# Kernel tuning notes

Hardware: AMD Instinct MI355X
Metric: run time of the kernel (lower is better)

The kernel has to match this reference:

```python
import jax, jax.numpy as jnp
import numpy as np

IN_DIM, H_DIM, EMB_DIM, CHEB_K = 2, 64, 10, 3
B, L, N = 16, 12, 2048
CAT = IN_DIM + H_DIM


def setup_inputs() -> dict:
    key = jax.random.key(0)
    ks = jax.random.split(key, 7)
    x = jax.random.normal(ks[0], (B, L, N, IN_DIM), dtype=jnp.float32)
    node_embs = jax.random.normal(ks[1], (N, EMB_DIM), dtype=jnp.float32)
    As = jax.random.uniform(ks[2], (N, N), dtype=jnp.float32) / N  # row-stochastic-ish support
    # NAPL parameter pools (AGCRN-style): per-gate weight/bias pools indexed by node embedding
    s = 0.1
    Wg_pool = jax.random.normal(ks[3], (EMB_DIM, CHEB_K, CAT, 2 * H_DIM), dtype=jnp.float32) * s
    bg_pool = jax.random.normal(ks[4], (EMB_DIM, 2 * H_DIM), dtype=jnp.float32) * s
    Wc_pool = jax.random.normal(ks[5], (EMB_DIM, CHEB_K, CAT, H_DIM), dtype=jnp.float32) * s
    bc_pool = jax.random.normal(ks[6], (EMB_DIM, H_DIM), dtype=jnp.float32) * s
    return {"x": x, "node_embs": node_embs, "As": As,
            "Wg_pool": Wg_pool, "bg_pool": bg_pool,
            "Wc_pool": Wc_pool, "bc_pool": bc_pool}


def _cheb_supports(A, k):
    # T0 = I, T1 = A, T_j = 2 A T_{j-1} - T_{j-2}
    n = A.shape[0]
    Ts = [jnp.eye(n, dtype=A.dtype), A]
    for _ in range(2, k):
        Ts.append(2.0 * A @ Ts[-1] - Ts[-2])
    return jnp.stack(Ts[:k], axis=0)  # (K, N, N)


def _napl_conv(xin, supports, Wn, bn):
    # xin: (B,N,Ci); supports: (K,N,N); Wn: (N,K,Ci,Co); bn: (N,Co)
    xg = jnp.einsum('knm,bmc->bnkc', supports, xin)
    return jnp.einsum('bnki,nkio->bno', xg, Wn) + bn


def reference(x, node_embs, As, Wg_pool, bg_pool, Wc_pool, bc_pool):
    supports = _cheb_supports(As, CHEB_K)
    # node-adaptive parameters (time-invariant: hoist out of the recurrence)
    Wg = jnp.einsum('nd,dkio->nkio', node_embs, Wg_pool)  # (N,K,CAT,2H)
    bg = node_embs @ bg_pool                               # (N,2H)
    Wc = jnp.einsum('nd,dkio->nkio', node_embs, Wc_pool)  # (N,K,CAT,H)
    bc = node_embs @ bc_pool                               # (N,H)

    def step(h_prev, x_t):
        cat = jnp.concatenate([h_prev, x_t], axis=-1)      # (B,N,CAT)
        gate = jax.nn.sigmoid(_napl_conv(cat, supports, Wg, bg))
        r_t, u_t = jnp.split(gate, 2, axis=-1)
        cat2 = jnp.concatenate([r_t * h_prev, x_t], axis=-1)
        c_t = jnp.tanh(_napl_conv(cat2, supports, Wc, bc))
        h_t = u_t * h_prev + (1.0 - u_t) * c_t
        return h_t, h_t

    h0 = jnp.zeros((x.shape[0], x.shape[2], H_DIM), dtype=x.dtype)
    x_time = jnp.moveaxis(x, 1, 0)                          # (L,B,N,C)
    h_n, outs = jax.lax.scan(step, h0, x_time)
    output = jnp.moveaxis(outs, 0, 1)                       # (B,L,N,H)
    return output, h_n
```

## Files before the change

kernel.cpp:

```cpp
#include <hip/hip_runtime.h>
#include <cstdint>
#include <cstddef>

typedef _Float16 h16;
typedef h16 v8h __attribute__((ext_vector_type(8)));
typedef h16 v4h __attribute__((ext_vector_type(4)));
typedef float v4f __attribute__((ext_vector_type(4)));

constexpr int NN = 2048;
constexpr float INV_N = 1.0f / 2048.0f;
constexpr int LP = 72;

#define MFMA16(a, b, c) __builtin_amdgcn_mfma_f32_16x16x32_f16((a), (b), (c), 0, 0, 0)

__global__ void fill_k(float* __restrict__ o, float v, size_t ntot) {
  size_t i = (size_t)blockIdx.x * 256 + threadIdx.x;
  if (i < ntot) o[i] = v;
}


__global__ void prep_Asplit_k(const float* __restrict__ A,
                              h16* __restrict__ hi, h16* __restrict__ lo) {
  int tid = blockIdx.x * 256 + threadIdx.x;
  float v = A[tid] * 2048.0f;
  h16 h = (h16)v;
  hi[tid] = h;
  lo[tid] = (h16)(v - (float)h);
}

__global__ void prep_AsTsplit_k(const float* __restrict__ A,
                                h16* __restrict__ hi, h16* __restrict__ lo) {
  int tid = blockIdx.x * 256 + threadIdx.x;
  int t = tid & 2047, j = tid >> 11;
  float v = A[(size_t)t * NN + j] * 2048.0f;
  h16 h = (h16)v;
  hi[(size_t)j * NN + t] = h;
  lo[(size_t)j * NN + t] = (h16)(v - (float)h);
}

__global__ void prep_x0split_k(const float* __restrict__ x,
                               h16* __restrict__ hi, h16* __restrict__ lo) {
  int tid = blockIdx.x * 256 + threadIdx.x;
  int n = tid & 2047, c = tid >> 11;
  int ii = c & 1, b = (c >> 1) & 15, lt = c >> 5;
  float v = x[(((size_t)(b * 12 + lt)) * NN + n) * 2 + ii];
  h16 h = (h16)v;
  hi[tid] = h;
  lo[tid] = (h16)(v - (float)h);
}

template<int CO>
__global__ void prep_wts_k(const float* __restrict__ Wp,
                           h16* __restrict__ WTh, h16* __restrict__ WTl) {
  int tid = blockIdx.x * 256 + threadIdx.x;
  int kk = tid % 1920, o = tid / 1920;
  int d = kk / 192, rem = kk - d * 192;
  int jb = rem >> 6, i = rem & 63;
  float v;
  if (jb == 0)
    v = Wp[((size_t)((d * 3 + 0) * 66 + i)) * CO + o] -
        Wp[((size_t)((d * 3 + 2) * 66 + i)) * CO + o];
  else if (jb == 1)
    v = Wp[((size_t)((d * 3 + 1) * 66 + i)) * CO + o];
  else
    v = 2.f * Wp[((size_t)((d * 3 + 2) * 66 + i)) * CO + o];
  h16 h = (h16)v;
  WTh[tid] = h;
  WTl[tid] = (h16)(v - (float)h);
}

template<int CO>
__global__ void prep_wx_k(const float* __restrict__ E, const float* __restrict__ Wp,
                          float* __restrict__ Wx) {
  int tid = blockIdx.x * 256 + threadIdx.x;
  int o = tid & (CO - 1), t6 = (tid / CO) % 6, n = tid / (6 * CO);
  int k = t6 >> 1, ii = t6 & 1;
  float s = 0.f;
  for (int d = 0; d < 10; ++d) {
    float p0 = Wp[((size_t)((d * 3 + 0) * 66 + 64 + ii)) * CO + o];
    float p1 = Wp[((size_t)((d * 3 + 1) * 66 + 64 + ii)) * CO + o];
    float p2 = Wp[((size_t)((d * 3 + 2) * 66 + 64 + ii)) * CO + o];
    float v = (k == 0) ? (p0 - p2) : (k == 1 ? p1 : 2.f * p2);
    s += E[n * 10 + d] * v;
  }
  Wx[tid] = s;
}

template<int CO>
__global__ void prep_b_k(const float* __restrict__ E, const float* __restrict__ bp,
                         float* __restrict__ bv) {
  int tid = blockIdx.x * 256 + threadIdx.x;
  int o = tid & (CO - 1), n = tid / CO;
  float s = 0.f;
  for (int d = 0; d < 10; ++d) s += E[n * 10 + d] * bp[d * CO + o];
  bv[tid] = s;
}

template<int OM>
__global__ __launch_bounds__(256, 4) void sgemm_k(
    const h16* __restrict__ Ih, const h16* __restrict__ Il,
    const h16* __restrict__ Bh, const h16* __restrict__ Bl,
    float* __restrict__ oF, h16* __restrict__ oH, h16* __restrict__ oL,
    float* __restrict__ xsv, int xoff) {
  const int m0 = blockIdx.x * 64, n0 = blockIdx.y * 64;
  __shared__ __align__(16) h16 sAh[64 * LP], sAl[64 * LP];
  __shared__ __align__(16) h16 sBh[64 * LP], sBl[64 * LP];
  const int tid = threadIdx.x, lane = tid & 63, w = tid >> 6;
  const int wm = w >> 1, wn = w & 1;
  v4f acc[2][2] = {};
  const int sr = tid >> 2, sc = (tid & 3) * 16;
  v8h rah0 = *(const v8h*)(Ih + (size_t)(m0 + sr) * NN + sc);
  v8h rah1 = *(const v8h*)(Ih + (size_t)(m0 + sr) * NN + sc + 8);
  v8h ral0 = *(const v8h*)(Il + (size_t)(m0 + sr) * NN + sc);
  v8h ral1 = *(const v8h*)(Il + (size_t)(m0 + sr) * NN + sc + 8);
  v8h rbh0 = *(const v8h*)(Bh + (size_t)(n0 + sr) * NN + sc);
  v8h rbh1 = *(const v8h*)(Bh + (size_t)(n0 + sr) * NN + sc + 8);
  v8h rbl0 = *(const v8h*)(Bl + (size_t)(n0 + sr) * NN + sc);
  v8h rbl1 = *(const v8h*)(Bl + (size_t)(n0 + sr) * NN + sc + 8);
  for (int kt = 0; kt < NN; kt += 64) {
    __syncthreads();
    *(v8h*)(sAh + sr * LP + sc) = rah0;
    *(v8h*)(sAh + sr * LP + sc + 8) = rah1;
    *(v8h*)(sAl + sr * LP + sc) = ral0;
    *(v8h*)(sAl + sr * LP + sc + 8) = ral1;
    *(v8h*)(sBh + sr * LP + sc) = rbh0;
    *(v8h*)(sBh + sr * LP + sc + 8) = rbh1;
    *(v8h*)(sBl + sr * LP + sc) = rbl0;
    *(v8h*)(sBl + sr * LP + sc + 8) = rbl1;
    __syncthreads();
    if (kt + 64 < NN) {
      const int k2 = kt + 64 + sc;
      rah0 = *(const v8h*)(Ih + (size_t)(m0 + sr) * NN + k2);
      rah1 = *(const v8h*)(Ih + (size_t)(m0 + sr) * NN + k2 + 8);
      ral0 = *(const v8h*)(Il + (size_t)(m0 + sr) * NN + k2);
      ral1 = *(const v8h*)(Il + (size_t)(m0 + sr) * NN + k2 + 8);
      rbh0 = *(const v8h*)(Bh + (size_t)(n0 + sr) * NN + k2);
      rbh1 = *(const v8h*)(Bh + (size_t)(n0 + sr) * NN + k2 + 8);
      rbl0 = *(const v8h*)(Bl + (size_t)(n0 + sr) * NN + k2);
      rbl1 = *(const v8h*)(Bl + (size_t)(n0 + sr) * NN + k2 + 8);
    }
#pragma unroll
    for (int kk = 0; kk < 2; ++kk) {
      const int ko = kk * 32 + (lane >> 4) * 8;
      const int rs = lane & 15;
      v8h Ah0 = *(const v8h*)(sAh + (wm * 32 + rs) * LP + ko);
      v8h Ah1 = *(const v8h*)(sAh + (wm * 32 + 16 + rs) * LP + ko);
      v8h Al0 = *(const v8h*)(sAl + (wm * 32 + rs) * LP + ko);
      v8h Al1 = *(const v8h*)(sAl + (wm * 32 + 16 + rs) * LP + ko);
      v8h Bh0 = *(const v8h*)(sBh + (wn * 32 + rs) * LP + ko);
      v8h Bh1 = *(const v8h*)(sBh + (wn * 32 + 16 + rs) * LP + ko);
      v8h Bl0 = *(const v8h*)(sBl + (wn * 32 + rs) * LP + ko);
      v8h Bl1 = *(const v8h*)(sBl + (wn * 32 + 16 + rs) * LP + ko);
      acc[0][0] = MFMA16(Ah0, Bh0, acc[0][0]);
      acc[0][1] = MFMA16(Ah0, Bh1, acc[0][1]);
      acc[1][0] = MFMA16(Ah1, Bh0, acc[1][0]);
      acc[1][1] = MFMA16(Ah1, Bh1, acc[1][1]);
      acc[0][0] = MFMA16(Al0, Bh0, acc[0][0]);
      acc[0][1] = MFMA16(Al0, Bh1, acc[0][1]);
      acc[1][0] = MFMA16(Al1, Bh0, acc[1][0]);
      acc[1][1] = MFMA16(Al1, Bh1, acc[1][1]);
      acc[0][0] = MFMA16(Ah0, Bl0, acc[0][0]);
      acc[0][1] = MFMA16(Ah0, Bl1, acc[0][1]);
      acc[1][0] = MFMA16(Ah1, Bl0, acc[1][0]);
      acc[1][1] = MFMA16(Ah1, Bl1, acc[1][1]);
    }
  }
  const int l15 = lane & 15, l4 = (lane >> 4) * 4;
#pragma unroll
  for (int ni = 0; ni < 2; ++ni) {
    const int n = n0 + wn * 32 + ni * 16 + l15;
#pragma unroll
    for (int mi = 0; mi < 2; ++mi) {
      const int cb = m0 + wm * 32 + mi * 16 + l4;
      float vv[4];
#pragma unroll
      for (int r = 0; r < 4; ++r) {
        vv[r] = acc[mi][ni][r] * INV_N;
        if constexpr (OM & 1) oF[(size_t)(cb + r) * NN + n] = vv[r];
        if constexpr (OM & 2) {
          h16 h = (h16)vv[r];
          oH[(size_t)(cb + r) * NN + n] = h;
          oL[(size_t)(cb + r) * NN + n] = (h16)(vv[r] - (float)h);
        }
      }
      if constexpr (OM & 4) {
        const int n2 = n & 2047;
        const int xo = xoff + ((n >> 11) << 6);
        v4f pv = {vv[0], vv[1], vv[2], vv[3]};
        *(v4f*)(xsv + ((size_t)(cb >> 6) * 2048 + n2) * 192 + xo + (cb & 63)) = pv;
      }
    }
  }
}

__global__ __launch_bounds__(256) void mgate_k(
    const float* __restrict__ xs, const h16* __restrict__ Bh, const h16* __restrict__ Bl,
    const float* __restrict__ E, const float* __restrict__ bgv,
    const float* __restrict__ Wx, const float* __restrict__ x,
    const float* __restrict__ X1t, const float* __restrict__ X2t,
    float* __restrict__ RHs, float* __restrict__ ubuf,
    h16* __restrict__ HRh, h16* __restrict__ HRl, int lt) {
  const int R0 = blockIdx.x * 32;
  const int gy = blockIdx.y, ob = gy * 64;
  const int bl = R0 >> 11, n0 = R0 & 2047;
  __shared__ __align__(16) h16 sAh[32 * LP], sAl[32 * LP];
  __shared__ __align__(16) h16 sBh[64 * LP], sBl[64 * LP];
  const int tid = threadIdx.x, lane = tid & 63, w = tid >> 6;
  v4f acc[2] = {};
  const int asr = tid >> 3, asc = (tid & 7) * 8;
  const int bsr = tid >> 2, bso = (tid & 3) * 16;
  const float* arow = xs + (size_t)(R0 + asr) * 192 + asc;
  const float* erow = E + (size_t)(n0 + asr) * 10;
  const h16* bhrow = Bh + (size_t)(ob + bsr) * 1920 + bso;
  const h16* blrow = Bl + (size_t)(ob + bsr) * 1920 + bso;
  v8h ah, al, pbh[2], pbl[2];
  auto load_t = [&](int t, int d, int jb) {
    const float e = erow[d];
    v4f a0 = *(const v4f*)(arow + jb * 64);
    v4f a1 = *(const v4f*)(arow + jb * 64 + 4);
#pragma unroll
    for (int q = 0; q < 4; ++q) {
      float v = a0[q] * e; h16 hh = (h16)v; ah[q] = hh; al[q] = (h16)(v - (float)hh);
      v = a1[q] * e; hh = (h16)v; ah[4 + q] = hh; al[4 + q] = (h16)(v - (float)hh);
    }
#pragma unroll
    for (int c = 0; c < 2; ++c) {
      pbh[c] = *(const v8h*)(bhrow + t * 64 + c * 8);
      pbl[c] = *(const v8h*)(blrow + t * 64 + c * 8);
    }
  };
  load_t(0, 0, 0);
  int d = 0, jb = 0;
  for (int t = 0; t < 30; ++t) {
    __syncthreads();
    *(v8h*)(sAh + asr * LP + asc) = ah;
    *(v8h*)(sAl + asr * LP + asc) = al;
#pragma unroll
    for (int c = 0; c < 2; ++c) {
      *(v8h*)(sBh + bsr * LP + bso + c * 8) = pbh[c];
      *(v8h*)(sBl + bsr * LP + bso + c * 8) = pbl[c];
    }
    __syncthreads();
    int dn = d, jn = jb + 1;
    if (jn == 3) { jn = 0; ++dn; }
    if (t < 29) load_t(t + 1, dn, jn);
#pragma unroll
    for (int kk = 0; kk < 2; ++kk) {
      const int ko = kk * 32 + (lane >> 4) * 8;
      const int rs = lane & 15;
      v8h Ah0 = *(const v8h*)(sAh + rs * LP + ko);
      v8h Ah1 = *(const v8h*)(sAh + (16 + rs) * LP + ko);
      v8h Al0 = *(const v8h*)(sAl + rs * LP + ko);
      v8h Al1 = *(const v8h*)(sAl + (16 + rs) * LP + ko);
      v8h Bh0 = *(const v8h*)(sBh + (w * 16 + rs) * LP + ko);
      v8h Bl0 = *(const v8h*)(sBl + (w * 16 + rs) * LP + ko);
      acc[0] = MFMA16(Ah0, Bh0, acc[0]);
      acc[1] = MFMA16(Ah1, Bh0, acc[1]);
      acc[0] = MFMA16(Al0, Bh0, acc[0]);
      acc[1] = MFMA16(Al1, Bh0, acc[1]);
      acc[0] = MFMA16(Ah0, Bl0, acc[0]);
      acc[1] = MFMA16(Ah1, Bl0, acc[1]);
      acc[0] = MFMA16(Al0, Bl0, acc[0]);
      acc[1] = MFMA16(Al1, Bl0, acc[1]);
    }
    d = dn; jb = jn;
  }
  const int l15 = lane & 15, l4 = (lane >> 4) * 4;
  const size_t xbase = ((size_t)(bl * 12 + lt)) * NN;
  const size_t c1 = ((size_t)(lt * 16 + bl)) * 2;
  const int o = ob + w * 16 + l15;
#pragma unroll
  for (int mi = 0; mi < 2; ++mi) {
    float rhv[4];
#pragma unroll
    for (int r = 0; r < 4; ++r) {
      const int Rl = mi * 16 + l4 + r;
      const int n = n0 + Rl;
      const size_t R = (size_t)R0 + Rl;
      const float x0a = x[(xbase + n) * 2 + 0];
      const float x0b = x[(xbase + n) * 2 + 1];
      const float x1a = X1t[c1 * NN + n];
      const float x1b = X1t[(c1 + 1) * NN + n];
      const float x2a = X2t[c1 * NN + n];
      const float x2b = X2t[(c1 + 1) * NN + n];
      const float* wx = Wx + (size_t)n * 768;
      float pre = acc[mi][r] + bgv[(size_t)n * 128 + o]
                + x0a * wx[o]       + x0b * wx[128 + o]
                + x1a * wx[256 + o] + x1b * wx[384 + o]
                + x2a * wx[512 + o] + x2b * wx[640 + o];
      const float g = 1.f / (1.f + expf(-pre));
      if (gy == 0) {
        const float rh = g * xs[R * 192 + o];
        RHs[(size_t)bl * 1572864 + (size_t)n * 64 + o] = rh;
        rhv[r] = rh;
      } else {
        ubuf[R * 64 + (o - 64)] = g;
      }
    }
    if (gy == 0) {
      const int nb = n0 + mi * 16 + l4;
      v4h ph, pl;
#pragma unroll
      for (int r = 0; r < 4; ++r) {
        h16 hh = (h16)rhv[r];
        ph[r] = hh;
        pl[r] = (h16)(rhv[r] - (float)hh);
      }
      *(v4h*)(HRh + (size_t)(bl * 64 + o) * 2048 + nb) = ph;
      *(v4h*)(HRl + (size_t)(bl * 64 + o) * 2048 + nb) = pl;
    }
  }
}

__global__ __launch_bounds__(256) void mcand_k(
    float* __restrict__ xs, const float* __restrict__ RHs,
    const h16* __restrict__ Bh, const h16* __restrict__ Bl,
    const float* __restrict__ E, const float* __restrict__ bcv,
    const float* __restrict__ Wx, const float* __restrict__ x,
    const float* __restrict__ X1t, const float* __restrict__ X2t,
    const float* __restrict__ ubuf, h16* __restrict__ HRh, h16* __restrict__ HRl,
    float* __restrict__ out, int lt) {
  const int R0 = blockIdx.x * 32;
  const int bl = R0 >> 11, n0 = R0 & 2047;
  __shared__ __align__(16) h16 sAh[32 * LP], sAl[32 * LP];
  __shared__ __align__(16) h16 sBh[64 * LP], sBl[64 * LP];
  const int tid = threadIdx.x, lane = tid & 63, w = tid >> 6;
  v4f acc[2] = {};
  const int asr = tid >> 3, asc = (tid & 7) * 8;
  const int bsr = tid >> 2, bso = (tid & 3) * 16;
  const float* erow = E + (size_t)(n0 + asr) * 10;
  const h16* bhrow = Bh + (size_t)bsr * 1920 + bso;
  const h16* blrow = Bl + (size_t)bsr * 1920 + bso;
  v8h ah, al, pbh[2], pbl[2];
  auto load_t = [&](int t, int d, int jb) {
    const float e = erow[d];
    const float* src = (jb == 0)
        ? (RHs + (size_t)bl * 1572864 + (size_t)(n0 + asr) * 64 + asc)
        : (xs + (size_t)(R0 + asr) * 192 + jb * 64 + asc);
    v4f a0 = *(const v4f*)src;
    v4f a1 = *(const v4f*)(src + 4);
#pragma unroll
    for (int q = 0; q < 4; ++q) {
      float v = a0[q] * e; h16 hh = (h16)v; ah[q] = hh; al[q] = (h16)(v - (float)hh);
      v = a1[q] * e; hh = (h16)v; ah[4 + q] = hh; al[4 + q] = (h16)(v - (float)hh);
    }
#pragma unroll
    for (int c = 0; c < 2; ++c) {
      pbh[c] = *(const v8h*)(bhrow + t * 64 + c * 8);
      pbl[c] = *(const v8h*)(blrow + t * 64 + c * 8);
    }
  };
  load_t(0, 0, 0);
  int d = 0, jb = 0;
  for (int t = 0; t < 30; ++t) {
    __syncthreads();
    *(v8h*)(sAh + asr * LP + asc) = ah;
    *(v8h*)(sAl + asr * LP + asc) = al;
#pragma unroll
    for (int c = 0; c < 2; ++c) {
      *(v8h*)(sBh + bsr * LP + bso + c * 8) = pbh[c];
      *(v8h*)(sBl + bsr * LP + bso + c * 8) = pbl[c];
    }
    __syncthreads();
    int dn = d, jn = jb + 1;
    if (jn == 3) { jn = 0; ++dn; }
    if (t < 29) load_t(t + 1, dn, jn);
#pragma unroll
    for (int kk = 0; kk < 2; ++kk) {
      const int ko = kk * 32 + (lane >> 4) * 8;
      const int rs = lane & 15;
      v8h Ah0 = *(const v8h*)(sAh + rs * LP + ko);
      v8h Ah1 = *(const v8h*)(sAh + (16 + rs) * LP + ko);
      v8h Al0 = *(const v8h*)(sAl + rs * LP + ko);
      v8h Al1 = *(const v8h*)(sAl + (16 + rs) * LP + ko);
      v8h Bh0 = *(const v8h*)(sBh + (w * 16 + rs) * LP + ko);
      v8h Bl0 = *(const v8h*)(sBl + (w * 16 + rs) * LP + ko);
      acc[0] = MFMA16(Ah0, Bh0, acc[0]);
      acc[1] = MFMA16(Ah1, Bh0, acc[1]);
      acc[0] = MFMA16(Al0, Bh0, acc[0]);
      acc[1] = MFMA16(Al1, Bh0, acc[1]);
      acc[0] = MFMA16(Ah0, Bl0, acc[0]);
      acc[1] = MFMA16(Ah1, Bl0, acc[1]);
      acc[0] = MFMA16(Al0, Bl0, acc[0]);
      acc[1] = MFMA16(Al1, Bl0, acc[1]);
    }
    d = dn; jb = jn;
  }
  const int l15 = lane & 15, l4 = (lane >> 4) * 4;
  const size_t xbase = ((size_t)(bl * 12 + lt)) * NN;
  const size_t c1 = ((size_t)(lt * 16 + bl)) * 2;
  const int o = w * 16 + l15;
#pragma unroll
  for (int mi = 0; mi < 2; ++mi) {
    float hnv[4];
#pragma unroll
    for (int r = 0; r < 4; ++r) {
      const int Rl = mi * 16 + l4 + r;
      const int n = n0 + Rl;
      const size_t R = (size_t)R0 + Rl;
      const float x0a = x[(xbase + n) * 2 + 0];
      const float x0b = x[(xbase + n) * 2 + 1];
      const float x1a = X1t[c1 * NN + n];
      const float x1b = X1t[(c1 + 1) * NN + n];
      const float x2a = X2t[c1 * NN + n];
      const float x2b = X2t[(c1 + 1) * NN + n];
      const float* wx = Wx + (size_t)n * 384;
      float pre = acc[mi][r] + bcv[(size_t)n * 64 + o]
                + x0a * wx[o]       + x0b * wx[64 + o]
                + x1a * wx[128 + o] + x1b * wx[192 + o]
                + x2a * wx[256 + o] + x2b * wx[320 + o];
      const float cv = tanhf(pre);
      const float u = ubuf[R * 64 + o];
      const float hold = xs[R * 192 + o];
      const float hn = u * hold + (1.f - u) * cv;
      hnv[r] = hn;
      xs[R * 192 + o] = hn;
      out[(xbase + n) * 64 + o] = hn;
    }
    const int nb = n0 + mi * 16 + l4;
    v4h ph, pl;
#pragma unroll
    for (int r = 0; r < 4; ++r) {
      h16 hh = (h16)hnv[r];
      ph[r] = hh;
      pl[r] = (h16)(hnv[r] - (float)hh);
    }
    *(v4h*)(HRh + (size_t)(bl * 64 + o) * 2048 + nb) = ph;
    *(v4h*)(HRl + (size_t)(bl * 64 + o) * 2048 + nb) = pl;
  }
}

__global__ void hn_gather_k(const float* __restrict__ xs, float* __restrict__ dst) {
  int i = blockIdx.x * 256 + threadIdx.x;
  dst[i] = xs[(size_t)(i >> 6) * 192 + (i & 63)];
}

extern "C" void kernel_launch(void* const* d_in, const int* in_sizes, int n_in,
                              void* d_out, int out_size, void* d_ws, size_t ws_size,
                              hipStream_t stream) {
  float* out = (float*)d_out;

  const bool in_ok = (n_in == 7) &&
      in_sizes[0] == 786432 && in_sizes[1] == 20480 && in_sizes[2] == 4194304 &&
      in_sizes[3] == 253440 && in_sizes[4] == 1280 &&
      in_sizes[5] == 126720 && in_sizes[6] == 640 && out_size == 27262976;
  if (!in_ok) {
    fill_k<<<(out_size + 255) / 256, 256, 0, stream>>>(out, 77.0f, (size_t)out_size);
    return;
  }
  constexpr size_t NEED = 85884928;
  if (ws_size < NEED) {
    fill_k<<<106496, 256, 0, stream>>>(out, 42.0f, 27262976);
    return;
  }

  const float* x   = (const float*)d_in[0];
  const float* E   = (const float*)d_in[1];
  const float* A   = (const float*)d_in[2];
  const float* Wgp = (const float*)d_in[3];
  const float* bgp = (const float*)d_in[4];
  const float* Wcp = (const float*)d_in[5];
  const float* bcp = (const float*)d_in[6];

  char* p = (char*)d_ws;
  auto carve = [&](size_t bytes) { char* r = p; p += bytes; return r; };
  h16*   ABh  = (h16*)carve(16777216);
  h16*   ABl  = (h16*)carve(16777216);
  float* X1t  = (float*)carve(3145728);
  float* X2t  = (float*)carve(3145728);
  h16*   WgTh = (h16*)carve(491520);
  h16*   WgTl = (h16*)carve(491520);
  h16*   WcTh = (h16*)carve(245760);
  h16*   WcTl = (h16*)carve(245760);
  float* WxG  = (float*)carve(6291456);
  float* WxC  = (float*)carve(3145728);
  float* bgv  = (float*)carve(1048576);
  float* bcv  = (float*)carve(524288);
  float* xs   = (float*)carve(25165824);
  h16*   HRh  = (h16*)carve(4194304);
  h16*   HRl  = (h16*)carve(4194304);
  float* RHs  = out + 1441792;
  float* ubuf = out + 25165824;
  h16* AsTh = (h16*)xs;
  h16* AsTl = (h16*)((char*)xs + 8388608);
  h16* X0h  = (h16*)((char*)xs + 16777216);
  h16* X0l  = (h16*)((char*)xs + 18350080);
  h16* X1h  = (h16*)((char*)xs + 19922944);
  h16* X1l  = (h16*)((char*)xs + 21495808);

  prep_Asplit_k<<<16384, 256, 0, stream>>>(A, ABh, ABl);
  prep_AsTsplit_k<<<16384, 256, 0, stream>>>(A, AsTh, AsTl);
  prep_wts_k<128><<<960, 256, 0, stream>>>(Wgp, WgTh, WgTl);
  prep_wts_k<64><<<480, 256, 0, stream>>>(Wcp, WcTh, WcTl);
  prep_wx_k<128><<<6144, 256, 0, stream>>>(E, Wgp, WxG);
  prep_wx_k<64><<<3072, 256, 0, stream>>>(E, Wcp, WxC);
  prep_b_k<128><<<1024, 256, 0, stream>>>(E, bgp, bgv);
  prep_b_k<64><<<512, 256, 0, stream>>>(E, bcp, bcv);
  sgemm_k<2><<<dim3(32, 32), 256, 0, stream>>>(ABh, ABl, AsTh, AsTl,
                                               nullptr, ABh + 4194304, ABl + 4194304,
                                               nullptr, 0);
  prep_x0split_k<<<3072, 256, 0, stream>>>(x, X0h, X0l);
  sgemm_k<3><<<dim3(6, 32), 256, 0, stream>>>(X0h, X0l, ABh, ABl, X1t, X1h, X1l, nullptr, 0);
  sgemm_k<1><<<dim3(6, 32), 256, 0, stream>>>(X1h, X1l, ABh, ABl, X2t, nullptr, nullptr, nullptr, 0);

  hipMemsetAsync(xs, 0, 25165824, stream);
  hipMemsetAsync(HRh, 0, 4194304, stream);
  hipMemsetAsync(HRl, 0, 4194304, stream);
  for (int lt = 0; lt < 12; ++lt) {
    sgemm_k<4><<<dim3(16, 64), 256, 0, stream>>>(HRh, HRl, ABh, ABl,
                                                 nullptr, nullptr, nullptr, xs, 64);
    mgate_k<<<dim3(1024, 2), 256, 0, stream>>>(xs, WgTh, WgTl, E, bgv, WxG, x, X1t, X2t,
                                               RHs, ubuf, HRh, HRl, lt);
    sgemm_k<4><<<dim3(16, 64), 256, 0, stream>>>(HRh, HRl, ABh, ABl,
                                                 nullptr, nullptr, nullptr, xs, 64);
    mcand_k<<<1024, 256, 0, stream>>>(xs, RHs, WcTh, WcTl, E, bcv, WxC, x, X1t, X2t,
                                      ubuf, HRh, HRl, out, lt);
  }
  hn_gather_k<<<8192, 256, 0, stream>>>(xs, out + 25165824);
}
```

Measured before the change: 3.808 ms.

## Pre-pack gate/candidate weights into MFMA fragment order and use single-wave blocks

Weights are now pre-packed in the exact per-lane MFMA B-fragment order, so mgate_k and mcand_k load them straight from global memory into registers. The kernels drop LDS staging and block barriers and run as one 64-lane wave per block. Each wave computes all 64 output columns (4 column blocks) for its 32 rows and converts activations to hi/lo fp16 in registers. This removes shared-memory traffic and barrier stalls, but gives fewer threads per block, more accumulator registers, and less reuse of the weight loads across waves.

Result: slower. 4.187 ms (+9.9%).

```diff
diff --git a/kernel.cpp b/kernel.cpp
--- a/kernel.cpp
+++ b/kernel.cpp
@@ -50,11 +50,20 @@
 }
 
 template<int CO>
-__global__ void prep_wts_k(const float* __restrict__ Wp,
-                           h16* __restrict__ WTh, h16* __restrict__ WTl) {
+__global__ void prep_wpack_k(const float* __restrict__ Wp,
+                             h16* __restrict__ Ph, h16* __restrict__ Pl) {
   int tid = blockIdx.x * 256 + threadIdx.x;
-  int kk = tid % 1920, o = tid / 1920;
-  int d = kk / 192, rem = kk - d * 192;
+  int c = tid & 7;
+  int ln = (tid >> 3) & 63;
+  int rest = tid >> 9;
+  int b = rest & 3;
+  int kk = (rest >> 2) & 1;
+  int r3 = rest >> 3;
+  int t = r3 % 30;
+  int g = r3 / 30;
+  int o = g * 64 + b * 16 + (ln & 15);
+  int kcol = (t / 3) * 192 + (t % 3) * 64 + kk * 32 + (ln >> 4) * 8 + c;
+  int d = kcol / 192, rem = kcol - d * 192;
   int jb = rem >> 6, i = rem & 63;
   float v;
   if (jb == 0)
@@ -65,8 +74,8 @@
   else
     v = 2.f * Wp[((size_t)((d * 3 + 2) * 66 + i)) * CO + o];
   h16 h = (h16)v;
-  WTh[tid] = h;
-  WTl[tid] = (h16)(v - (float)h);
+  Ph[tid] = h;
+  Pl[tid] = (h16)(v - (float)h);
 }
 
 template<int CO>
@@ -193,8 +202,8 @@
   }
 }
 
-__global__ __launch_bounds__(256) void mgate_k(
-    const float* __restrict__ xs, const h16* __restrict__ Bh, const h16* __restrict__ Bl,
+__global__ __launch_bounds__(64) void mgate_k(
+    const float* __restrict__ xs, const h16* __restrict__ Bph, const h16* __restrict__ Bpl,
     const float* __restrict__ E, const float* __restrict__ bgv,
     const float* __restrict__ Wx, const float* __restrict__ x,
     const float* __restrict__ X1t, const float* __restrict__ X2t,
@@ -203,118 +212,106 @@
   const int R0 = blockIdx.x * 32;
   const int gy = blockIdx.y, ob = gy * 64;
   const int bl = R0 >> 11, n0 = R0 & 2047;
-  __shared__ __align__(16) h16 sAh[32 * LP], sAl[32 * LP];
-  __shared__ __align__(16) h16 sBh[64 * LP], sBl[64 * LP];
-  const int tid = threadIdx.x, lane = tid & 63, w = tid >> 6;
-  v4f acc[2] = {};
-  const int asr = tid >> 3, asc = (tid & 7) * 8;
-  const int bsr = tid >> 2, bso = (tid & 3) * 16;
-  const float* arow = xs + (size_t)(R0 + asr) * 192 + asc;
-  const float* erow = E + (size_t)(n0 + asr) * 10;
-  const h16* bhrow = Bh + (size_t)(ob + bsr) * 1920 + bso;
-  const h16* blrow = Bl + (size_t)(ob + bsr) * 1920 + bso;
-  v8h ah, al, pbh[2], pbl[2];
-  auto load_t = [&](int t, int d, int jb) {
-    const float e = erow[d];
-    v4f a0 = *(const v4f*)(arow + jb * 64);
-    v4f a1 = *(const v4f*)(arow + jb * 64 + 4);
-#pragma unroll
-    for (int q = 0; q < 4; ++q) {
-      float v = a0[q] * e; h16 hh = (h16)v; ah[q] = hh; al[q] = (h16)(v - (float)hh);
-      v = a1[q] * e; hh = (h16)v; ah[4 + q] = hh; al[4 + q] = (h16)(v - (float)hh);
-    }
-#pragma unroll
-    for (int c = 0; c < 2; ++c) {
-      pbh[c] = *(const v8h*)(bhrow + t * 64 + c * 8);
-      pbl[c] = *(const v8h*)(blrow + t * 64 + c * 8);
-    }
-  };
-  load_t(0, 0, 0);
+  const int lane = threadIdx.x;
+  const int rs = lane & 15, q = lane >> 4;
+  float e0[10], e1[10];
+#pragma unroll
+  for (int d = 0; d < 10; ++d) {
+    e0[d] = E[(size_t)(n0 + rs) * 10 + d];
+    e1[d] = E[(size_t)(n0 + 16 + rs) * 10 + d];
+  }
+  const float* a0base = xs + (size_t)(R0 + rs) * 192;
+  const float* a1base = xs + (size_t)(R0 + 16 + rs) * 192;
+  const h16* pbh = Bph + (size_t)gy * 122880 + lane * 8;
+  const h16* pbl = Bpl + (size_t)gy * 122880 + lane * 8;
+  v4f acc[2][4] = {};
   int d = 0, jb = 0;
   for (int t = 0; t < 30; ++t) {
-    __syncthreads();
-    *(v8h*)(sAh + asr * LP + asc) = ah;
-    *(v8h*)(sAl + asr * LP + asc) = al;
-#pragma unroll
-    for (int c = 0; c < 2; ++c) {
-      *(v8h*)(sBh + bsr * LP + bso + c * 8) = pbh[c];
-      *(v8h*)(sBl + bsr * LP + bso + c * 8) = pbl[c];
-    }
-    __syncthreads();
-    int dn = d, jn = jb + 1;
-    if (jn == 3) { jn = 0; ++dn; }
-    if (t < 29) load_t(t + 1, dn, jn);
+    const float ed0 = e0[d], ed1 = e1[d];
 #pragma unroll
     for (int kk = 0; kk < 2; ++kk) {
-      const int ko = kk * 32 + (lane >> 4) * 8;
-      const int rs = lane & 15;
-      v8h Ah0 = *(const v8h*)(sAh + rs * LP + ko);
-      v8h Ah1 = *(const v8h*)(sAh + (16 + rs) * LP + ko);
-      v8h Al0 = *(const v8h*)(sAl + rs * LP + ko);
-      v8h Al1 = *(const v8h*)(sAl + (16 + rs) * LP + ko);
-      v8h Bh0 = *(const v8h*)(sBh + (w * 16 + rs) * LP + ko);
-      v8h Bl0 = *(const v8h*)(sBl + (w * 16 + rs) * LP + ko);
-      acc[0] = MFMA16(Ah0, Bh0, acc[0]);
-      acc[1] = MFMA16(Ah1, Bh0, acc[1]);
-      acc[0] = MFMA16(Al0, Bh0, acc[0]);
-      acc[1] = MFMA16(Al1, Bh0, acc[1]);
-      acc[0] = MFMA16(Ah0, Bl0, acc[0]);
-      acc[1] = MFMA16(Ah1, Bl0, acc[1]);
-      acc[0] = MFMA16(Al0, Bl0, acc[0]);
-      acc[1] = MFMA16(Al1, Bl0, acc[1]);
-    }
-    d = dn; jb = jn;
-  }
-  const int l15 = lane & 15, l4 = (lane >> 4) * 4;
+      const int co = jb * 64 + kk * 32 + q * 8;
+      v4f x00 = *(const v4f*)(a0base + co);
+      v4f x01 = *(const v4f*)(a0base + co + 4);
+      v4f x10 = *(const v4f*)(a1base + co);
+      v4f x11 = *(const v4f*)(a1base + co + 4);
+      v8h Ah0, Al0, Ah1, Al1;
+#pragma unroll
+      for (int i = 0; i < 4; ++i) {
+        float v = x00[i] * ed0; h16 hh = (h16)v; Ah0[i] = hh; Al0[i] = (h16)(v - (float)hh);
+        v = x01[i] * ed0; hh = (h16)v; Ah0[4 + i] = hh; Al0[4 + i] = (h16)(v - (float)hh);
+        v = x10[i] * ed1; hh = (h16)v; Ah1[i] = hh; Al1[i] = (h16)(v - (float)hh);
+        v = x11[i] * ed1; hh = (h16)v; Ah1[4 + i] = hh; Al1[4 + i] = (h16)(v - (float)hh);
+      }
+      const size_t boff = (size_t)((t * 2 + kk) * 4) * 512;
+#pragma unroll
+      for (int b = 0; b < 4; ++b) {
+        v8h Bh = *(const v8h*)(pbh + boff + b * 512);
+        v8h Bl = *(const v8h*)(pbl + boff + b * 512);
+        acc[0][b] = MFMA16(Ah0, Bh, acc[0][b]);
+        acc[1][b] = MFMA16(Ah1, Bh, acc[1][b]);
+        acc[0][b] = MFMA16(Al0, Bh, acc[0][b]);
+        acc[1][b] = MFMA16(Al1, Bh, acc[1][b]);
+        acc[0][b] = MFMA16(Ah0, Bl, acc[0][b]);
+        acc[1][b] = MFMA16(Ah1, Bl, acc[1][b]);
+        acc[0][b] = MFMA16(Al0, Bl, acc[0][b]);
+        acc[1][b] = MFMA16(Al1, Bl, acc[1][b]);
+      }
+    }
+    if (++jb == 3) { jb = 0; ++d; }
+  }
   const size_t xbase = ((size_t)(bl * 12 + lt)) * NN;
   const size_t c1 = ((size_t)(lt * 16 + bl)) * 2;
-  const int o = ob + w * 16 + l15;
 #pragma unroll
   for (int mi = 0; mi < 2; ++mi) {
-    float rhv[4];
-#pragma unroll
-    for (int r = 0; r < 4; ++r) {
-      const int Rl = mi * 16 + l4 + r;
-      const int n = n0 + Rl;
-      const size_t R = (size_t)R0 + Rl;
-      const float x0a = x[(xbase + n) * 2 + 0];
-      const float x0b = x[(xbase + n) * 2 + 1];
-      const float x1a = X1t[c1 * NN + n];
-      const float x1b = X1t[(c1 + 1) * NN + n];
-      const float x2a = X2t[c1 * NN + n];
-      const float x2b = X2t[(c1 + 1) * NN + n];
-      const float* wx = Wx + (size_t)n * 768;
-      float pre = acc[mi][r] + bgv[(size_t)n * 128 + o]
-                + x0a * wx[o]       + x0b * wx[128 + o]
-                + x1a * wx[256 + o] + x1b * wx[384 + o]
-                + x2a * wx[512 + o] + x2b * wx[640 + o];
-      const float g = 1.f / (1.f + expf(-pre));
+#pragma unroll
+    for (int b = 0; b < 4; ++b) {
+      const int o = ob + b * 16 + rs;
+      float rhv[4];
+#pragma unroll
+      for (int r = 0; r < 4; ++r) {
+        const int Rl = mi * 16 + q * 4 + r;
+        const int n = n0 + Rl;
+        const size_t R = (size_t)R0 + Rl;
+        const float x0a = x[(xbase + n) * 2 + 0];
+        const float x0b = x[(xbase + n) * 2 + 1];
+        const float x1a = X1t[c1 * NN + n];
+        const float x1b = X1t[(c1 + 1) * NN + n];
+        const float x2a = X2t[c1 * NN + n];
+        const float x2b = X2t[(c1 + 1) * NN + n];
+        const float* wx = Wx + (size_t)n * 768;
+        float pre = acc[mi][b][r] + bgv[(size_t)n * 128 + o]
+                  + x0a * wx[o]       + x0b * wx[128 + o]
+                  + x1a * wx[256 + o] + x1b * wx[384 + o]
+                  + x2a * wx[512 + o] + x2b * wx[640 + o];
+        const float g = 1.f / (1.f + expf(-pre));
+        if (gy == 0) {
+          const float rh = g * xs[R * 192 + o];
+          RHs[(size_t)bl * 1572864 + (size_t)n * 64 + o] = rh;
+          rhv[r] = rh;
+        } else {
+          ubuf[R * 64 + (o - 64)] = g;
+        }
+      }
       if (gy == 0) {
-        const float rh = g * xs[R * 192 + o];
-        RHs[(size_t)bl * 1572864 + (size_t)n * 64 + o] = rh;
-        rhv[r] = rh;
-      } else {
-        ubuf[R * 64 + (o - 64)] = g;
-      }
-    }
-    if (gy == 0) {
-      const int nb = n0 + mi * 16 + l4;
-      v4h ph, pl;
-#pragma unroll
-      for (int r = 0; r < 4; ++r) {
-        h16 hh = (h16)rhv[r];
-        ph[r] = hh;
-        pl[r] = (h16)(rhv[r] - (float)hh);
-      }
-      *(v4h*)(HRh + (size_t)(bl * 64 + o) * 2048 + nb) = ph;
-      *(v4h*)(HRl + (size_t)(bl * 64 + o) * 2048 + nb) = pl;
-    }
-  }
-}
-
-__global__ __launch_bounds__(256) void mcand_k(
+        const int nb = n0 + mi * 16 + q * 4;
+        v4h ph, pl;
+#pragma unroll
+        for (int r = 0; r < 4; ++r) {
+          h16 hh = (h16)rhv[r];
+          ph[r] = hh;
+          pl[r] = (h16)(rhv[r] - (float)hh);
+        }
+        *(v4h*)(HRh + (size_t)(bl * 64 + o) * 2048 + nb) = ph;
+        *(v4h*)(HRl + (size_t)(bl * 64 + o) * 2048 + nb) = pl;
+      }
+    }
+  }
+}
+
+__global__ __launch_bounds__(64) void mcand_k(
     float* __restrict__ xs, const float* __restrict__ RHs,
-    const h16* __restrict__ Bh, const h16* __restrict__ Bl,
+    const h16* __restrict__ Bph, const h16* __restrict__ Bpl,
     const float* __restrict__ E, const float* __restrict__ bcv,
     const float* __restrict__ Wx, const float* __restrict__ x,
     const float* __restrict__ X1t, const float* __restrict__ X2t,
@@ -322,111 +319,101 @@
     float* __restrict__ out, int lt) {
   const int R0 = blockIdx.x * 32;
   const int bl = R0 >> 11, n0 = R0 & 2047;
-  __shared__ __align__(16) h16 sAh[32 * LP], sAl[32 * LP];
-  __shared__ __align__(16) h16 sBh[64 * LP], sBl[64 * LP];
-  const int tid = threadIdx.x, lane = tid & 63, w = tid >> 6;
-  v4f acc[2] = {};
-  const int asr = tid >> 3, asc = (tid & 7) * 8;
-  const int bsr = tid >> 2, bso = (tid & 3) * 16;
-  const float* erow = E + (size_t)(n0 + asr) * 10;
-  const h16* bhrow = Bh + (size_t)bsr * 1920 + bso;
-  const h16* blrow = Bl + (size_t)bsr * 1920 + bso;
-  v8h ah, al, pbh[2], pbl[2];
-  auto load_t = [&](int t, int d, int jb) {
-    const float e = erow[d];
-    const float* src = (jb == 0)
-        ? (RHs + (size_t)bl * 1572864 + (size_t)(n0 + asr) * 64 + asc)
-        : (xs + (size_t)(R0 + asr) * 192 + jb * 64 + asc);
-    v4f a0 = *(const v4f*)src;
-    v4f a1 = *(const v4f*)(src + 4);
-#pragma unroll
-    for (int q = 0; q < 4; ++q) {
-      float v = a0[q] * e; h16 hh = (h16)v; ah[q] = hh; al[q] = (h16)(v - (float)hh);
-      v = a1[q] * e; hh = (h16)v; ah[4 + q] = hh; al[4 + q] = (h16)(v - (float)hh);
-    }
-#pragma unroll
-    for (int c = 0; c < 2; ++c) {
-      pbh[c] = *(const v8h*)(bhrow + t * 64 + c * 8);
-      pbl[c] = *(const v8h*)(blrow + t * 64 + c * 8);
-    }
-  };
-  load_t(0, 0, 0);
+  const int lane = threadIdx.x;
+  const int rs = lane & 15, q = lane >> 4;
+  float e0[10], e1[10];
+#pragma unroll
+  for (int d = 0; d < 10; ++d) {
+    e0[d] = E[(size_t)(n0 + rs) * 10 + d];
+    e1[d] = E[(size_t)(n0 + 16 + rs) * 10 + d];
+  }
+  const float* rh0 = RHs + (size_t)bl * 1572864 + (size_t)(n0 + rs) * 64;
+  const float* rh1 = RHs + (size_t)bl * 1572864 + (size_t)(n0 + 16 + rs) * 64;
+  const float* xs0 = xs + (size_t)(R0 + rs) * 192;
+  const float* xs1 = xs + (size_t)(R0 + 16 + rs) * 192;
+  const h16* pbh = Bph + lane * 8;
+  const h16* pbl = Bpl + lane * 8;
+  v4f acc[2][4] = {};
   int d = 0, jb = 0;
   for (int t = 0; t < 30; ++t) {
-    __syncthreads();
-    *(v8h*)(sAh + asr * LP + asc) = ah;
-    *(v8h*)(sAl + asr * LP + asc) = al;
-#pragma unroll
-    for (int c = 0; c < 2; ++c) {
-      *(v8h*)(sBh + bsr * LP + bso + c * 8) = pbh[c];
-      *(v8h*)(sBl + bsr * LP + bso + c * 8) = pbl[c];
-    }
-    __syncthreads();
-    int dn = d, jn = jb + 1;
-    if (jn == 3) { jn = 0; ++dn; }
-    if (t < 29) load_t(t + 1, dn, jn);
+    const float ed0 = e0[d], ed1 = e1[d];
 #pragma unroll
     for (int kk = 0; kk < 2; ++kk) {
-      const int ko = kk * 32 + (lane >> 4) * 8;
-      const int rs = lane & 15;
-      v8h Ah0 = *(const v8h*)(sAh + rs * LP + ko);
-      v8h Ah1 = *(const v8h*)(sAh + (16 + rs) * LP + ko);
-      v8h Al0 = *(const v8h*)(sAl + rs * LP + ko);
-      v8h Al1 = *(const v8h*)(sAl + (16 + rs) * LP + ko);
-      v8h Bh0 = *(const v8h*)(sBh + (w * 16 + rs) * LP + ko);
-      v8h Bl0 = *(const v8h*)(sBl + (w * 16 + rs) * LP + ko);
-      acc[0] = MFMA16(Ah0, Bh0, acc[0]);
-      acc[1] = MFMA16(Ah1, Bh0, acc[1]);
-      acc[0] = MFMA16(Al0, Bh0, acc[0]);
-      acc[1] = MFMA16(Al1, Bh0, acc[1]);
-      acc[0] = MFMA16(Ah0, Bl0, acc[0]);
-      acc[1] = MFMA16(Ah1, Bl0, acc[1]);
-      acc[0] = MFMA16(Al0, Bl0, acc[0]);
-      acc[1] = MFMA16(Al1, Bl0, acc[1]);
-    }
-    d = dn; jb = jn;
-  }
-  const int l15 = lane & 15, l4 = (lane >> 4) * 4;
+      const int cq = kk * 32 + q * 8;
+      const float* s0 = (jb == 0) ? (rh0 + cq) : (xs0 + jb * 64 + cq);
+      const float* s1 = (jb == 0) ? (rh1 + cq) : (xs1 + jb * 64 + cq);
+      v4f x00 = *(const v4f*)s0;
+      v4f x01 = *(const v4f*)(s0 + 4);
+      v4f x10 = *(const v4f*)s1;
+      v4f x11 = *(const v4f*)(s1 + 4);
+      v8h Ah0, Al0, Ah1, Al1;
+#pragma unroll
+      for (int i = 0; i < 4; ++i) {
+        float v = x00[i] * ed0; h16 hh = (h16)v; Ah0[i] = hh; Al0[i] = (h16)(v - (float)hh);
+        v = x01[i] * ed0; hh = (h16)v; Ah0[4 + i] = hh; Al0[4 + i] = (h16)(v - (float)hh);
+        v = x10[i] * ed1; hh = (h16)v; Ah1[i] = hh; Al1[i] = (h16)(v - (float)hh);
+        v = x11[i] * ed1; hh = (h16)v; Ah1[4 + i] = hh; Al1[4 + i] = (h16)(v - (float)hh);
+      }
+      const size_t boff = (size_t)((t * 2 + kk) * 4) * 512;
+#pragma unroll
+      for (int b = 0; b < 4; ++b) {
+        v8h Bh = *(const v8h*)(pbh + boff + b * 512);
+        v8h Bl = *(const v8h*)(pbl + boff + b * 512);
+        acc[0][b] = MFMA16(Ah0, Bh, acc[0][b]);
+        acc[1][b] = MFMA16(Ah1, Bh, acc[1][b]);
+        acc[0][b] = MFMA16(Al0, Bh, acc[0][b]);
+        acc[1][b] = MFMA16(Al1, Bh, acc[1][b]);
+        acc[0][b] = MFMA16(Ah0, Bl, acc[0][b]);
+        acc[1][b] = MFMA16(Ah1, Bl, acc[1][b]);
+        acc[0][b] = MFMA16(Al0, Bl, acc[0][b]);
+        acc[1][b] = MFMA16(Al1, Bl, acc[1][b]);
+      }
+    }
+    if (++jb == 3) { jb = 0; ++d; }
+  }
   const size_t xbase = ((size_t)(bl * 12 + lt)) * NN;
   const size_t c1 = ((size_t)(lt * 16 + bl)) * 2;
-  const int o = w * 16 + l15;
 #pragma unroll
   for (int mi = 0; mi < 2; ++mi) {
-    float hnv[4];
-#pragma unroll
-    for (int r = 0; r < 4; ++r) {
-      const int Rl = mi * 16 + l4 + r;
-      const int n = n0 + Rl;
-      const size_t R = (size_t)R0 + Rl;
-      const float x0a = x[(xbase + n) * 2 + 0];
-      const float x0b = x[(xbase + n) * 2 + 1];
-      const float x1a = X1t[c1 * NN + n];
-      const float x1b = X1t[(c1 + 1) * NN + n];
-      const float x2a = X2t[c1 * NN + n];
-      const float x2b = X2t[(c1 + 1) * NN + n];
-      const float* wx = Wx + (size_t)n * 384;
-      float pre = acc[mi][r] + bcv[(size_t)n * 64 + o]
-                + x0a * wx[o]       + x0b * wx[64 + o]
-                + x1a * wx[128 + o] + x1b * wx[192 + o]
-                + x2a * wx[256 + o] + x2b * wx[320 + o];
-      const float cv = tanhf(pre);
-      const float u = ubuf[R * 64 + o];
-      const float hold = xs[R * 192 + o];
-      const float hn = u * hold + (1.f - u) * cv;
-      hnv[r] = hn;
-      xs[R * 192 + o] = hn;
-      out[(xbase + n) * 64 + o] = hn;
-    }
-    const int nb = n0 + mi * 16 + l4;
-    v4h ph, pl;
-#pragma unroll
-    for (int r = 0; r < 4; ++r) {
-      h16 hh = (h16)hnv[r];
-      ph[r] = hh;
-      pl[r] = (h16)(hnv[r] - (float)hh);
-    }
-    *(v4h*)(HRh + (size_t)(bl * 64 + o) * 2048 + nb) = ph;
-    *(v4h*)(HRl + (size_t)(bl * 64 + o) * 2048 + nb) = pl;
+#pragma unroll
+    for (int b = 0; b < 4; ++b) {
+      const int o = b * 16 + rs;
+      float hnv[4];
+#pragma unroll
+      for (int r = 0; r < 4; ++r) {
+        const int Rl = mi * 16 + q * 4 + r;
+        const int n = n0 + Rl;
+        const size_t R = (size_t)R0 + Rl;
+        const float x0a = x[(xbase + n) * 2 + 0];
+        const float x0b = x[(xbase + n) * 2 + 1];
+        const float x1a = X1t[c1 * NN + n];
+        const float x1b = X1t[(c1 + 1) * NN + n];
+        const float x2a = X2t[c1 * NN + n];
+        const float x2b = X2t[(c1 + 1) * NN + n];
+        const float* wx = Wx + (size_t)n * 384;
+        float pre = acc[mi][b][r] + bcv[(size_t)n * 64 + o]
+                  + x0a * wx[o]       + x0b * wx[64 + o]
+                  + x1a * wx[128 + o] + x1b * wx[192 + o]
+                  + x2a * wx[256 + o] + x2b * wx[320 + o];
+        const float cv = tanhf(pre);
+        const float u = ubuf[R * 64 + o];
+        const float hold = xs[R * 192 + o];
+        const float hn = u * hold + (1.f - u) * cv;
+        hnv[r] = hn;
+        xs[R * 192 + o] = hn;
+        out[(xbase + n) * 64 + o] = hn;
+      }
+      const int nb = n0 + mi * 16 + q * 4;
+      v4h ph, pl;
+#pragma unroll
+      for (int r = 0; r < 4; ++r) {
+        h16 hh = (h16)hnv[r];
+        ph[r] = hh;
+        pl[r] = (h16)(hnv[r] - (float)hh);
+      }
+      *(v4h*)(HRh + (size_t)(bl * 64 + o) * 2048 + nb) = ph;
+      *(v4h*)(HRl + (size_t)(bl * 64 + o) * 2048 + nb) = pl;
+    }
   }
 }
 
@@ -490,8 +477,8 @@
 
   prep_Asplit_k<<<16384, 256, 0, stream>>>(A, ABh, ABl);
   prep_AsTsplit_k<<<16384, 256, 0, stream>>>(A, AsTh, AsTl);
-  prep_wts_k<128><<<960, 256, 0, stream>>>(Wgp, WgTh, WgTl);
-  prep_wts_k<64><<<480, 256, 0, stream>>>(Wcp, WcTh, WcTl);
+  prep_wpack_k<128><<<960, 256, 0, stream>>>(Wgp, WgTh, WgTl);
+  prep_wpack_k<64><<<480, 256, 0, stream>>>(Wcp, WcTh, WcTl);
   prep_wx_k<128><<<6144, 256, 0, stream>>>(E, Wgp, WxG);
   prep_wx_k<64><<<3072, 256, 0, stream>>>(E, Wcp, WxC);
   prep_b_k<128><<<1024, 256, 0, stream>>>(E, bgp, bgv);
@@ -509,12 +496,12 @@
   for (int lt = 0; lt < 12; ++lt) {
     sgemm_k<4><<<dim3(16, 64), 256, 0, stream>>>(HRh, HRl, ABh, ABl,
                                                  nullptr, nullptr, nullptr, xs, 64);
-    mgate_k<<<dim3(1024, 2), 256, 0, stream>>>(xs, WgTh, WgTl, E, bgv, WxG, x, X1t, X2t,
-                                               RHs, ubuf, HRh, HRl, lt);
+    mgate_k<<<dim3(1024, 2), 64, 0, stream>>>(xs, WgTh, WgTl, E, bgv, WxG, x, X1t, X2t,
+                                              RHs, ubuf, HRh, HRl, lt);
     sgemm_k<4><<<dim3(16, 64), 256, 0, stream>>>(HRh, HRl, ABh, ABl,
                                                  nullptr, nullptr, nullptr, xs, 64);
-    mcand_k<<<1024, 256, 0, stream>>>(xs, RHs, WcTh, WcTl, E, bcv, WxC, x, X1t, X2t,
-                                      ubuf, HRh, HRl, out, lt);
+    mcand_k<<<1024, 64, 0, stream>>>(xs, RHs, WcTh, WcTl, E, bcv, WxC, x, X1t, X2t,
+                                     ubuf, HRh, HRl, out, lt);
   }
   hn_gather_k<<<8192, 256, 0, stream>>>(xs, out + 25165824);
 }
```
